# Optimization experiments

Measured on AMD Instinct MI355X. Metric: run time of the kernel, lower is better.

## Reference

```python
import jax, jax.numpy as jnp
import numpy as np

N_NODES = 100000
N_EDGES = 3200000
D_NODE = 5            # per-node feature dim
D_IN = 2 * D_NODE     # 10, MLP input dim
D_HID = D_IN * 5      # 50, HIDDEN_DIM_MULTIPLIER = 5


def setup_inputs() -> dict:
    key = jax.random.key(0)
    ks = jax.random.split(key, 8)
    x = jax.random.normal(ks[0], (N_NODES, D_NODE), dtype=jnp.float32)
    edge_index = jax.random.randint(ks[1], (2, N_EDGES), 0, N_NODES, dtype=jnp.int64)
    s1 = 1.0 / np.sqrt(D_IN)
    s2 = 1.0 / np.sqrt(D_HID)
    W1 = jax.random.uniform(ks[2], (D_IN, D_HID), jnp.float32, -s1, s1)
    b1 = jax.random.uniform(ks[3], (D_HID,), jnp.float32, -s1, s1)
    W2 = jax.random.uniform(ks[4], (D_HID, D_HID), jnp.float32, -s2, s2)
    b2 = jax.random.uniform(ks[5], (D_HID,), jnp.float32, -s2, s2)
    W3 = jax.random.uniform(ks[6], (D_HID, 1), jnp.float32, -s2, s2)
    b3 = jax.random.uniform(ks[7], (1,), jnp.float32, -s2, s2)
    return {"x": x, "edge_index": edge_index, "W1": W1, "b1": b1,
            "W2": W2, "b2": b2, "W3": W3, "b3": b3}


def reference(x, edge_index, W1, b1, W2, b2, W3, b3):
    # gather src/tgt node features and concat -> [E, 2*D_NODE]
    ef = jnp.concatenate([x[edge_index[0]], x[edge_index[1]]], axis=-1)
    h = jax.nn.relu(ef @ W1 + b1)
    h = jax.nn.relu(h @ W2 + b2)
    return jax.nn.sigmoid(h @ W3 + b3)  # [E, 1]
```

## Files before the change

kernel.cpp:

```cpp
#include <hip/hip_runtime.h>
#include <hip/hip_bf16.h>

typedef short bf16x8 __attribute__((ext_vector_type(8)));
typedef float f32x4  __attribute__((ext_vector_type(4)));

union fragU { f32x4 f; bf16x8 b; uint4 q; uint u[4]; };

__device__ inline ushort f2bf(float f) {
    union { float f; uint u; } v; v.f = f;
    uint r = (v.u + 0x7FFFu + ((v.u >> 16) & 1u)) >> 16;
    return (ushort)r;
}
__device__ inline uint packbf(float a, float b) {
    return (uint)f2bf(a) | ((uint)f2bf(b) << 16);
}
__device__ inline uint cvtpk(float lo, float hi) {
    uint r;
    asm("v_cvt_pk_bf16_f32 %0, %1, %2" : "=v"(r) : "v"(lo), "v"(hi));
    return r;
}

__global__ __launch_bounds__(256) void pack_x_kernel(
    const float* __restrict__ x, uint4* __restrict__ xp, int N)
{
    int i = blockIdx.x * blockDim.x + threadIdx.x;
    if (i > N) return;
    uint4 o = {0u, 0u, 0u, 0u};
    if (i < N) {
        const float* r = x + (size_t)i * 5;
        o.x = packbf(r[0], r[1]);
        o.y = packbf(r[2], r[3]);
        o.z = packbf(r[4], 1.0f);
    }
    xp[i] = o;
}

__global__ __launch_bounds__(64) void pack_w_kernel(
    const float* __restrict__ W1, const float* __restrict__ b1,
    const float* __restrict__ W2, const float* __restrict__ b2,
    const float* __restrict__ W3, uint4* __restrict__ tab)
{
    const int lane = threadIdx.x;
    const int c = lane & 15;
    const int g = lane >> 4;

    union { ushort s[8]; uint4 q; } u;
    #pragma unroll
    for (int mt = 0; mt < 4; ++mt) {
        #pragma unroll
        for (int d = 0; d < 8; ++d) {
            int k = 8 * g + d;
            int j = 16 * mt + c;
            float v = 0.f;
            if (j < 50) {
                if (k < 5)                 v = W1[k * 50 + j];
                else if (k == 5)           v = b1[j];
                else if (k >= 8 && k < 13) v = W1[(k - 3) * 50 + j];
            } else if (j == 50 && k == 5)  v = 1.0f;
            u.s[d] = f2bf(v);
        }
        tab[mt * 64 + lane] = u.q;
    }
    #pragma unroll
    for (int t = 0; t < 2; ++t) {
        #pragma unroll
        for (int mt = 0; mt < 4; ++mt) {
            #pragma unroll
            for (int d = 0; d < 8; ++d) {
                int hid1 = 16 * (2 * t + (d >> 2)) + 4 * g + (d & 3);
                int j    = 16 * mt + c;
                float v = 0.f;
                if (j < 50) {
                    if (hid1 < 50)       v = W2[hid1 * 50 + j];
                    else if (hid1 == 50) v = b2[j];
                }
                u.s[d] = f2bf(v);
            }
            tab[(4 + t * 4 + mt) * 64 + lane] = u.q;
        }
    }
    #pragma unroll
    for (int t = 0; t < 2; ++t) {
        #pragma unroll
        for (int d = 0; d < 8; ++d) {
            int hid = 16 * (2 * t + (d >> 2)) + 4 * g + (d & 3);
            float v = (c == 0 && hid < 50) ? W3[hid] : 0.f;
            u.s[d] = f2bf(v);
        }
        tab[(12 + t) * 64 + lane] = u.q;
    }
}

__global__ __launch_bounds__(256, 4) void edge_mlp_mfma9(
    const uint4* __restrict__ xp,
    const uint4* __restrict__ wtab,
    const int* __restrict__ ei,
    const float* __restrict__ b3,
    float* __restrict__ out, int E, int num_tiles)
{
    const int tid  = threadIdx.x;
    const int w    = tid >> 6;
    const int lane = tid & 63;
    const int c    = lane & 15;
    const int g    = lane >> 4;
    const int G    = gridDim.x;

    fragU w1f[4], w2f[8], w3f[2];
    #pragma unroll
    for (int i = 0; i < 4; ++i) w1f[i].q = wtab[i * 64 + lane];
    #pragma unroll
    for (int i = 0; i < 8; ++i) w2f[i].q = wtab[(4 + i) * 64 + lane];
    #pragma unroll
    for (int i = 0; i < 2; ++i) w3f[i].q = wtab[(12 + i) * 64 + lane];
    asm volatile("" :
        "+v"(w1f[0].f), "+v"(w1f[1].f), "+v"(w1f[2].f), "+v"(w1f[3].f),
        "+v"(w2f[0].f), "+v"(w2f[1].f), "+v"(w2f[2].f), "+v"(w2f[3].f),
        "+v"(w2f[4].f), "+v"(w2f[5].f), "+v"(w2f[6].f), "+v"(w2f[7].f),
        "+v"(w3f[0].f), "+v"(w3f[1].f));

    const float b3s = b3[0];

    auto LOAD_IDX = [&](int bt_) -> int {
        int bc = (bt_ < num_tiles) ? bt_ : (num_tiles - 1);
        int v = 0;
        if (g < 2) {
            int e = bc * 64 + w * 16 + c;
            if (e >= E) e = 0;
            v = ei[(size_t)g * (size_t)E + (size_t)e];
        }
        return v;
    };
    auto GATHER = [&](int idx) -> fragU {
        fragU a;
        uint4 q = {0u, 0u, 0u, 0u};
        if (g < 2) q = xp[idx];
        a.q = q;
        return a;
    };

    int bt = blockIdx.x;
    if (bt >= num_tiles) return;

    fragU fC = GATHER(LOAD_IDX(bt));
    int idxN = LOAD_IDX(bt + G);

    for (; bt < num_tiles; bt += G) {
        fragU fN = GATHER(idxN);
        idxN = LOAD_IDX(bt + 2 * G);

        f32x4 hT[4];
        #pragma unroll
        for (int mt = 0; mt < 4; ++mt) {
            f32x4 z = {0.f, 0.f, 0.f, 0.f};
            hT[mt] = __builtin_amdgcn_mfma_f32_16x16x32_bf16(w1f[mt].b, fC.b, z, 0, 0, 0);
        }
        fragU bB0, bB1;
        #pragma unroll
        for (int mt = 0; mt < 2; ++mt) {
            bB0.u[2*mt]   = cvtpk(fmaxf(hT[mt][0], 0.f),   fmaxf(hT[mt][1], 0.f));
            bB0.u[2*mt+1] = cvtpk(fmaxf(hT[mt][2], 0.f),   fmaxf(hT[mt][3], 0.f));
            bB1.u[2*mt]   = cvtpk(fmaxf(hT[2+mt][0], 0.f), fmaxf(hT[2+mt][1], 0.f));
            bB1.u[2*mt+1] = cvtpk(fmaxf(hT[2+mt][2], 0.f), fmaxf(hT[2+mt][3], 0.f));
        }

        f32x4 h2T[4];
        #pragma unroll
        for (int mt = 0; mt < 4; ++mt) {
            f32x4 z = {0.f, 0.f, 0.f, 0.f};
            h2T[mt] = __builtin_amdgcn_mfma_f32_16x16x32_bf16(w2f[mt].b,     bB0.b, z, 0, 0, 0);
            h2T[mt] = __builtin_amdgcn_mfma_f32_16x16x32_bf16(w2f[4 + mt].b, bB1.b, h2T[mt], 0, 0, 0);
        }
        fragU cB0, cB1;
        #pragma unroll
        for (int mt = 0; mt < 2; ++mt) {
            cB0.u[2*mt]   = cvtpk(fmaxf(h2T[mt][0], 0.f),   fmaxf(h2T[mt][1], 0.f));
            cB0.u[2*mt+1] = cvtpk(fmaxf(h2T[mt][2], 0.f),   fmaxf(h2T[mt][3], 0.f));
            cB1.u[2*mt]   = cvtpk(fmaxf(h2T[2+mt][0], 0.f), fmaxf(h2T[2+mt][1], 0.f));
            cB1.u[2*mt+1] = cvtpk(fmaxf(h2T[2+mt][2], 0.f), fmaxf(h2T[2+mt][3], 0.f));
        }

        f32x4 z3 = {0.f, 0.f, 0.f, 0.f};
        f32x4 o3 = __builtin_amdgcn_mfma_f32_16x16x32_bf16(w3f[0].b, cB0.b, z3, 0, 0, 0);
        o3 = __builtin_amdgcn_mfma_f32_16x16x32_bf16(w3f[1].b, cB1.b, o3, 0, 0, 0);

        if (g == 0) {
            int e = bt * 64 + w * 16 + c;
            if (e < E) {
                float ex = __expf(-(o3[0] + b3s));
                out[e] = __builtin_amdgcn_rcpf(1.f + ex);
            }
        }

        fC = fN;
    }
}

extern "C" void kernel_launch(void* const* d_in, const int* in_sizes, int n_in,
                              void* d_out, int out_size, void* d_ws, size_t ws_size,
                              hipStream_t stream) {
    const float* x  = (const float*)d_in[0];
    const int*   ei = (const int*)d_in[1];
    const float* W1 = (const float*)d_in[2];
    const float* b1 = (const float*)d_in[3];
    const float* W2 = (const float*)d_in[4];
    const float* b2 = (const float*)d_in[5];
    const float* W3 = (const float*)d_in[6];
    const float* b3 = (const float*)d_in[7];
    float* out = (float*)d_out;

    int E = in_sizes[1] / 2;
    int N = in_sizes[0] / 5;

    uint4* wtab = (uint4*)d_ws;
    uint4* xp   = (uint4*)((char*)d_ws + 16384);

    pack_w_kernel<<<1, 64, 0, stream>>>(W1, b1, W2, b2, W3, wtab);
    pack_x_kernel<<<(N + 1 + 255) / 256, 256, 0, stream>>>(x, xp, N);

    int num_tiles = (E + 63) / 64;
    int grid = num_tiles < 2048 ? num_tiles : 2048;
    edge_mlp_mfma9<<<grid, 256, 0, stream>>>(xp, wtab, ei, b3, out, E, num_tiles);
}
```

Baseline: 77.29 us.

## Deepen gather prefetch pipeline to four tiles and use nontemporal index loads and stores

Replaces the single-tile-ahead prefetch with a four-slot rotating buffer, so each wavefront keeps several index loads and feature gathers in flight while it runs the MFMA chain on an earlier tile. The goal is to hide gather latency in this memory-bound edge MLP. Edge index loads and output stores also become nontemporal, so streamed data does not evict the gathered node table from cache. The cost is more live registers and some wasted compute on clamped tiles at the end of the grid-stride loop, since tail tiles past num_tiles are computed and then discarded by the bounds check.

```diff
diff --git a/kernel.cpp b/kernel.cpp
--- a/kernel.cpp
+++ b/kernel.cpp
@@ -91,7 +91,7 @@
     }
 }
 
-__global__ __launch_bounds__(256, 4) void edge_mlp_mfma9(
+__global__ __launch_bounds__(256, 4) void edge_mlp_mfma10(
     const uint4* __restrict__ xp,
     const uint4* __restrict__ wtab,
     const int* __restrict__ ei,
@@ -126,7 +126,7 @@
         if (g < 2) {
             int e = bc * 64 + w * 16 + c;
             if (e >= E) e = 0;
-            v = ei[(size_t)g * (size_t)E + (size_t)e];
+            v = __builtin_nontemporal_load(&ei[(size_t)g * (size_t)E + (size_t)e]);
         }
         return v;
     };
@@ -138,21 +138,12 @@
         return a;
     };
 
-    int bt = blockIdx.x;
-    if (bt >= num_tiles) return;
-
-    fragU fC = GATHER(LOAD_IDX(bt));
-    int idxN = LOAD_IDX(bt + G);
-
-    for (; bt < num_tiles; bt += G) {
-        fragU fN = GATHER(idxN);
-        idxN = LOAD_IDX(bt + 2 * G);
-
+    auto COMPUTE = [&](fragU aX, int T) {
         f32x4 hT[4];
         #pragma unroll
         for (int mt = 0; mt < 4; ++mt) {
             f32x4 z = {0.f, 0.f, 0.f, 0.f};
-            hT[mt] = __builtin_amdgcn_mfma_f32_16x16x32_bf16(w1f[mt].b, fC.b, z, 0, 0, 0);
+            hT[mt] = __builtin_amdgcn_mfma_f32_16x16x32_bf16(w1f[mt].b, aX.b, z, 0, 0, 0);
         }
         fragU bB0, bB1;
         #pragma unroll
@@ -162,7 +153,6 @@
             bB1.u[2*mt]   = cvtpk(fmaxf(hT[2+mt][0], 0.f), fmaxf(hT[2+mt][1], 0.f));
             bB1.u[2*mt+1] = cvtpk(fmaxf(hT[2+mt][2], 0.f), fmaxf(hT[2+mt][3], 0.f));
         }
-
         f32x4 h2T[4];
         #pragma unroll
         for (int mt = 0; mt < 4; ++mt) {
@@ -178,20 +168,40 @@
             cB1.u[2*mt]   = cvtpk(fmaxf(h2T[2+mt][0], 0.f), fmaxf(h2T[2+mt][1], 0.f));
             cB1.u[2*mt+1] = cvtpk(fmaxf(h2T[2+mt][2], 0.f), fmaxf(h2T[2+mt][3], 0.f));
         }
-
         f32x4 z3 = {0.f, 0.f, 0.f, 0.f};
         f32x4 o3 = __builtin_amdgcn_mfma_f32_16x16x32_bf16(w3f[0].b, cB0.b, z3, 0, 0, 0);
         o3 = __builtin_amdgcn_mfma_f32_16x16x32_bf16(w3f[1].b, cB1.b, o3, 0, 0, 0);
 
         if (g == 0) {
-            int e = bt * 64 + w * 16 + c;
+            int e = T * 64 + w * 16 + c;
             if (e < E) {
                 float ex = __expf(-(o3[0] + b3s));
-                out[e] = __builtin_amdgcn_rcpf(1.f + ex);
+                float sg = __builtin_amdgcn_rcpf(1.f + ex);
+                __builtin_nontemporal_store(sg, &out[e]);
             }
         }
-
-        fC = fN;
+    };
+
+    int bt = blockIdx.x;
+    if (bt >= num_tiles) return;
+
+    int idxB[4];
+    fragU fB[4];
+    #pragma unroll
+    for (int p = 0; p < 4; ++p) idxB[p] = LOAD_IDX(bt + p * G);
+    #pragma unroll
+    for (int p = 0; p < 4; ++p) fB[p] = GATHER(idxB[p]);
+    #pragma unroll
+    for (int p = 0; p < 4; ++p) idxB[p] = LOAD_IDX(bt + (p + 4) * G);
+
+    for (; bt < num_tiles; bt += 4 * G) {
+        #pragma unroll
+        for (int p = 0; p < 4; ++p) {
+            const int T = bt + p * G;
+            COMPUTE(fB[p], T);
+            fB[p] = GATHER(idxB[p]);
+            idxB[p] = LOAD_IDX(bt + (p + 8) * G);
+        }
     }
 }
 
@@ -219,5 +229,5 @@
 
     int num_tiles = (E + 63) / 64;
     int grid = num_tiles < 2048 ? num_tiles : 2048;
-    edge_mlp_mfma9<<<grid, 256, 0, stream>>>(xp, wtab, ei, b3, out, E, num_tiles);
-}
+    edge_mlp_mfma10<<<grid, 256, 0, stream>>>(xp, wtab, ei, b3, out, E, num_tiles);
+}
```

Result: faster. 73.18 us (-5.3%).

## Process eight edge subtiles per wave with vectorized nontemporal index loads

Applied to the files above, without the earlier changes.

Each block now handles 512 edges per iteration instead of 64. Each lane loads 8 contiguous edge indices with two 16-byte nontemporal loads, issues 8 independent feature gathers up front, then runs the MFMA MLP chain for each subtile. This is meant to raise memory-level parallelism and cut per-edge index-load instruction overhead. It also adds s_setprio around the MFMA section, nontemporal output stores, and lowers the occupancy hint to 3 blocks per CU, at the cost of more registers and strided output writes.

```diff
diff --git a/kernel.cpp b/kernel.cpp
--- a/kernel.cpp
+++ b/kernel.cpp
@@ -3,6 +3,7 @@
 
 typedef short bf16x8 __attribute__((ext_vector_type(8)));
 typedef float f32x4  __attribute__((ext_vector_type(4)));
+typedef int   i32x4  __attribute__((ext_vector_type(4)));
 
 union fragU { f32x4 f; bf16x8 b; uint4 q; uint u[4]; };
 
@@ -91,12 +92,12 @@
     }
 }
 
-__global__ __launch_bounds__(256, 4) void edge_mlp_mfma9(
+__global__ __launch_bounds__(256, 3) void edge_mlp_mfma11(
     const uint4* __restrict__ xp,
     const uint4* __restrict__ wtab,
     const int* __restrict__ ei,
     const float* __restrict__ b3,
-    float* __restrict__ out, int E, int num_tiles)
+    float* __restrict__ out, int E, int NB)
 {
     const int tid  = threadIdx.x;
     const int w    = tid >> 6;
@@ -119,79 +120,101 @@
         "+v"(w3f[0].f), "+v"(w3f[1].f));
 
     const float b3s = b3[0];
-
-    auto LOAD_IDX = [&](int bt_) -> int {
-        int bc = (bt_ < num_tiles) ? bt_ : (num_tiles - 1);
-        int v = 0;
+    const bool e_al = ((E & 3) == 0);
+
+    auto LOAD_IDX = [&](int bt_, i32x4& a, i32x4& b) {
+        a = i32x4{0, 0, 0, 0};
+        b = i32x4{0, 0, 0, 0};
+        int bc = (bt_ < NB) ? bt_ : (NB - 1);
+        int base = bc * 512 + w * 128;
         if (g < 2) {
-            int e = bc * 64 + w * 16 + c;
-            if (e >= E) e = 0;
-            v = ei[(size_t)g * (size_t)E + (size_t)e];
-        }
-        return v;
+            if (e_al && base + 128 <= E) {
+                const i32x4* p = (const i32x4*)(ei + (size_t)g * (size_t)E + base + c * 8);
+                a = __builtin_nontemporal_load(p);
+                b = __builtin_nontemporal_load(p + 1);
+            } else {
+                int t[8];
+                #pragma unroll
+                for (int jj = 0; jj < 8; ++jj) {
+                    int e = base + c * 8 + jj;
+                    if (e >= E) e = 0;
+                    t[jj] = ei[(size_t)g * (size_t)E + (size_t)e];
+                }
+                a = i32x4{t[0], t[1], t[2], t[3]};
+                b = i32x4{t[4], t[5], t[6], t[7]};
+            }
+        }
     };
-    auto GATHER = [&](int idx) -> fragU {
-        fragU a;
-        uint4 q = {0u, 0u, 0u, 0u};
-        if (g < 2) q = xp[idx];
-        a.q = q;
-        return a;
-    };
 
     int bt = blockIdx.x;
-    if (bt >= num_tiles) return;
-
-    fragU fC = GATHER(LOAD_IDX(bt));
-    int idxN = LOAD_IDX(bt + G);
-
-    for (; bt < num_tiles; bt += G) {
-        fragU fN = GATHER(idxN);
-        idxN = LOAD_IDX(bt + 2 * G);
-
-        f32x4 hT[4];
-        #pragma unroll
-        for (int mt = 0; mt < 4; ++mt) {
-            f32x4 z = {0.f, 0.f, 0.f, 0.f};
-            hT[mt] = __builtin_amdgcn_mfma_f32_16x16x32_bf16(w1f[mt].b, fC.b, z, 0, 0, 0);
-        }
-        fragU bB0, bB1;
-        #pragma unroll
-        for (int mt = 0; mt < 2; ++mt) {
-            bB0.u[2*mt]   = cvtpk(fmaxf(hT[mt][0], 0.f),   fmaxf(hT[mt][1], 0.f));
-            bB0.u[2*mt+1] = cvtpk(fmaxf(hT[mt][2], 0.f),   fmaxf(hT[mt][3], 0.f));
-            bB1.u[2*mt]   = cvtpk(fmaxf(hT[2+mt][0], 0.f), fmaxf(hT[2+mt][1], 0.f));
-            bB1.u[2*mt+1] = cvtpk(fmaxf(hT[2+mt][2], 0.f), fmaxf(hT[2+mt][3], 0.f));
-        }
-
-        f32x4 h2T[4];
-        #pragma unroll
-        for (int mt = 0; mt < 4; ++mt) {
-            f32x4 z = {0.f, 0.f, 0.f, 0.f};
-            h2T[mt] = __builtin_amdgcn_mfma_f32_16x16x32_bf16(w2f[mt].b,     bB0.b, z, 0, 0, 0);
-            h2T[mt] = __builtin_amdgcn_mfma_f32_16x16x32_bf16(w2f[4 + mt].b, bB1.b, h2T[mt], 0, 0, 0);
-        }
-        fragU cB0, cB1;
-        #pragma unroll
-        for (int mt = 0; mt < 2; ++mt) {
-            cB0.u[2*mt]   = cvtpk(fmaxf(h2T[mt][0], 0.f),   fmaxf(h2T[mt][1], 0.f));
-            cB0.u[2*mt+1] = cvtpk(fmaxf(h2T[mt][2], 0.f),   fmaxf(h2T[mt][3], 0.f));
-            cB1.u[2*mt]   = cvtpk(fmaxf(h2T[2+mt][0], 0.f), fmaxf(h2T[2+mt][1], 0.f));
-            cB1.u[2*mt+1] = cvtpk(fmaxf(h2T[2+mt][2], 0.f), fmaxf(h2T[2+mt][3], 0.f));
-        }
-
-        f32x4 z3 = {0.f, 0.f, 0.f, 0.f};
-        f32x4 o3 = __builtin_amdgcn_mfma_f32_16x16x32_bf16(w3f[0].b, cB0.b, z3, 0, 0, 0);
-        o3 = __builtin_amdgcn_mfma_f32_16x16x32_bf16(w3f[1].b, cB1.b, o3, 0, 0, 0);
-
-        if (g == 0) {
-            int e = bt * 64 + w * 16 + c;
-            if (e < E) {
-                float ex = __expf(-(o3[0] + b3s));
-                out[e] = __builtin_amdgcn_rcpf(1.f + ex);
-            }
-        }
-
-        fC = fN;
+    if (bt >= NB) return;
+
+    i32x4 iaC, ibC, iaN, ibN;
+    LOAD_IDX(bt, iaC, ibC);
+
+    for (; bt < NB; bt += G) {
+        LOAD_IDX(bt + G, iaN, ibN);
+
+        int idxs[8] = {iaC[0], iaC[1], iaC[2], iaC[3], ibC[0], ibC[1], ibC[2], ibC[3]};
+
+        fragU f[8];
+        #pragma unroll
+        for (int j = 0; j < 8; ++j) {
+            uint4 q = {0u, 0u, 0u, 0u};
+            if (g < 2) q = xp[idxs[j]];
+            f[j].q = q;
+        }
+
+        const int base = bt * 512 + w * 128;
+
+        #pragma unroll
+        for (int j = 0; j < 8; ++j) {
+            __builtin_amdgcn_s_setprio(1);
+            f32x4 hT[4];
+            #pragma unroll
+            for (int mt = 0; mt < 4; ++mt) {
+                f32x4 z = {0.f, 0.f, 0.f, 0.f};
+                hT[mt] = __builtin_amdgcn_mfma_f32_16x16x32_bf16(w1f[mt].b, f[j].b, z, 0, 0, 0);
+            }
+            fragU bB0, bB1;
+            #pragma unroll
+            for (int mt = 0; mt < 2; ++mt) {
+                bB0.u[2*mt]   = cvtpk(fmaxf(hT[mt][0], 0.f),   fmaxf(hT[mt][1], 0.f));
+                bB0.u[2*mt+1] = cvtpk(fmaxf(hT[mt][2], 0.f),   fmaxf(hT[mt][3], 0.f));
+                bB1.u[2*mt]   = cvtpk(fmaxf(hT[2+mt][0], 0.f), fmaxf(hT[2+mt][1], 0.f));
+                bB1.u[2*mt+1] = cvtpk(fmaxf(hT[2+mt][2], 0.f), fmaxf(hT[2+mt][3], 0.f));
+            }
+            f32x4 h2T[4];
+            #pragma unroll
+            for (int mt = 0; mt < 4; ++mt) {
+                f32x4 z = {0.f, 0.f, 0.f, 0.f};
+                h2T[mt] = __builtin_amdgcn_mfma_f32_16x16x32_bf16(w2f[mt].b,     bB0.b, z, 0, 0, 0);
+                h2T[mt] = __builtin_amdgcn_mfma_f32_16x16x32_bf16(w2f[4 + mt].b, bB1.b, h2T[mt], 0, 0, 0);
+            }
+            fragU cB0, cB1;
+            #pragma unroll
+            for (int mt = 0; mt < 2; ++mt) {
+                cB0.u[2*mt]   = cvtpk(fmaxf(h2T[mt][0], 0.f),   fmaxf(h2T[mt][1], 0.f));
+                cB0.u[2*mt+1] = cvtpk(fmaxf(h2T[mt][2], 0.f),   fmaxf(h2T[mt][3], 0.f));
+                cB1.u[2*mt]   = cvtpk(fmaxf(h2T[2+mt][0], 0.f), fmaxf(h2T[2+mt][1], 0.f));
+                cB1.u[2*mt+1] = cvtpk(fmaxf(h2T[2+mt][2], 0.f), fmaxf(h2T[2+mt][3], 0.f));
+            }
+            f32x4 z3 = {0.f, 0.f, 0.f, 0.f};
+            f32x4 o3 = __builtin_amdgcn_mfma_f32_16x16x32_bf16(w3f[0].b, cB0.b, z3, 0, 0, 0);
+            o3 = __builtin_amdgcn_mfma_f32_16x16x32_bf16(w3f[1].b, cB1.b, o3, 0, 0, 0);
+            __builtin_amdgcn_s_setprio(0);
+
+            if (g == 0) {
+                int e = base + c * 8 + j;
+                if (e < E) {
+                    float ex = __expf(-(o3[0] + b3s));
+                    float sg = __builtin_amdgcn_rcpf(1.f + ex);
+                    __builtin_nontemporal_store(sg, &out[e]);
+                }
+            }
+        }
+
+        iaC = iaN; ibC = ibN;
     }
 }
 
@@ -217,7 +240,7 @@
     pack_w_kernel<<<1, 64, 0, stream>>>(W1, b1, W2, b2, W3, wtab);
     pack_x_kernel<<<(N + 1 + 255) / 256, 256, 0, stream>>>(x, xp, N);
 
-    int num_tiles = (E + 63) / 64;
-    int grid = num_tiles < 2048 ? num_tiles : 2048;
-    edge_mlp_mfma9<<<grid, 256, 0, stream>>>(xp, wtab, ei, b3, out, E, num_tiles);
-}
+    int NB = (E + 511) / 512;
+    int grid = NB < 2048 ? NB : 2048;
+    edge_mlp_mfma11<<<grid, 256, 0, stream>>>(xp, wtab, ei, b3, out, E, NB);
+}
```

Result: faster. 75.60 us (-2.2%).

## Switch edge MLP to 32x32x16 MFMA tiles with permlane swap and FMA output layer

Applied to the files above, without the earlier changes.

Each wave now processes 32 edges per tile instead of 16, using 32x32x16 bf16 MFMA for layers 1 and 2. The layer-1 accumulators are reshaped into B operands with v_permlane32_swap rather than reused directly. The final 50->1 layer becomes a per-lane FMA dot product plus a cross-half shuffle, replacing two mostly zero MFMAs. This cuts wasted MFMA work and halves the index-load and gather instructions per edge, at the cost of more registers (occupancy hint lowered from 4 to 3) and added permute and FMA instructions.

```diff
diff --git a/kernel.cpp b/kernel.cpp
--- a/kernel.cpp
+++ b/kernel.cpp
@@ -3,6 +3,7 @@
 
 typedef short bf16x8 __attribute__((ext_vector_type(8)));
 typedef float f32x4  __attribute__((ext_vector_type(4)));
+typedef float f32x16 __attribute__((ext_vector_type(16)));
 
 union fragU { f32x4 f; bf16x8 b; uint4 q; uint u[4]; };
 
@@ -24,14 +25,13 @@
     const float* __restrict__ x, uint4* __restrict__ xp, int N)
 {
     int i = blockIdx.x * blockDim.x + threadIdx.x;
-    if (i > N) return;
-    uint4 o = {0u, 0u, 0u, 0u};
-    if (i < N) {
-        const float* r = x + (size_t)i * 5;
-        o.x = packbf(r[0], r[1]);
-        o.y = packbf(r[2], r[3]);
-        o.z = packbf(r[4], 1.0f);
-    }
+    if (i >= N) return;
+    const float* r = x + (size_t)i * 5;
+    uint4 o;
+    o.x = packbf(r[0], r[1]);
+    o.y = packbf(r[2], r[3]);
+    o.z = packbf(r[4], 1.0f);
+    o.w = 0u;
     xp[i] = o;
 }
 
@@ -41,16 +41,16 @@
     const float* __restrict__ W3, uint4* __restrict__ tab)
 {
     const int lane = threadIdx.x;
-    const int c = lane & 15;
-    const int g = lane >> 4;
+    const int col  = lane & 31;
+    const int hi   = lane >> 5;
 
     union { ushort s[8]; uint4 q; } u;
     #pragma unroll
-    for (int mt = 0; mt < 4; ++mt) {
+    for (int T = 0; T < 2; ++T) {
         #pragma unroll
         for (int d = 0; d < 8; ++d) {
-            int k = 8 * g + d;
-            int j = 16 * mt + c;
+            int k = 8 * hi + d;
+            int j = 32 * T + col;
             float v = 0.f;
             if (j < 50) {
                 if (k < 5)                 v = W1[k * 50 + j];
@@ -59,139 +59,139 @@
             } else if (j == 50 && k == 5)  v = 1.0f;
             u.s[d] = f2bf(v);
         }
-        tab[mt * 64 + lane] = u.q;
-    }
-    #pragma unroll
-    for (int t = 0; t < 2; ++t) {
-        #pragma unroll
-        for (int mt = 0; mt < 4; ++mt) {
+        tab[T * 64 + lane] = u.q;
+    }
+    #pragma unroll
+    for (int T = 0; T < 2; ++T) {
+        #pragma unroll
+        for (int s = 0; s < 4; ++s) {
             #pragma unroll
             for (int d = 0; d < 8; ++d) {
-                int hid1 = 16 * (2 * t + (d >> 2)) + 4 * g + (d & 3);
-                int j    = 16 * mt + c;
+                int kg = 16 * s + 8 * hi + d;
+                int j  = 32 * T + col;
                 float v = 0.f;
                 if (j < 50) {
-                    if (hid1 < 50)       v = W2[hid1 * 50 + j];
-                    else if (hid1 == 50) v = b2[j];
+                    if (kg < 50)       v = W2[kg * 50 + j];
+                    else if (kg == 50) v = b2[j];
                 }
                 u.s[d] = f2bf(v);
             }
-            tab[(4 + t * 4 + mt) * 64 + lane] = u.q;
-        }
-    }
-    #pragma unroll
-    for (int t = 0; t < 2; ++t) {
-        #pragma unroll
-        for (int d = 0; d < 8; ++d) {
-            int hid = 16 * (2 * t + (d >> 2)) + 4 * g + (d & 3);
-            float v = (c == 0 && hid < 50) ? W3[hid] : 0.f;
-            u.s[d] = f2bf(v);
-        }
-        tab[(12 + t) * 64 + lane] = u.q;
-    }
-}
-
-__global__ __launch_bounds__(256, 4) void edge_mlp_mfma9(
+            tab[(2 + T * 4 + s) * 64 + lane] = u.q;
+        }
+    }
+    union { float f[4]; uint4 q; } wq;
+    #pragma unroll
+    for (int T = 0; T < 2; ++T) {
+        #pragma unroll
+        for (int rq = 0; rq < 4; ++rq) {
+            #pragma unroll
+            for (int rr = 0; rr < 4; ++rr) {
+                int reg = 4 * rq + rr;
+                int row = (reg & 3) + 8 * (reg >> 2) + 4 * hi + 32 * T;
+                wq.f[rr] = (row < 50) ? W3[row] : 0.f;
+            }
+            tab[(10 + T * 4 + rq) * 64 + lane] = wq.q;
+        }
+    }
+}
+
+__global__ __launch_bounds__(256, 3) void edge_mlp_mfma12(
     const uint4* __restrict__ xp,
     const uint4* __restrict__ wtab,
     const int* __restrict__ ei,
     const float* __restrict__ b3,
-    float* __restrict__ out, int E, int num_tiles)
+    float* __restrict__ out, int E, int NT)
 {
     const int tid  = threadIdx.x;
     const int w    = tid >> 6;
     const int lane = tid & 63;
-    const int c    = lane & 15;
-    const int g    = lane >> 4;
+    const int col  = lane & 31;
+    const int hi   = lane >> 5;
     const int G    = gridDim.x;
 
-    fragU w1f[4], w2f[8], w3f[2];
-    #pragma unroll
-    for (int i = 0; i < 4; ++i) w1f[i].q = wtab[i * 64 + lane];
-    #pragma unroll
-    for (int i = 0; i < 8; ++i) w2f[i].q = wtab[(4 + i) * 64 + lane];
-    #pragma unroll
-    for (int i = 0; i < 2; ++i) w3f[i].q = wtab[(12 + i) * 64 + lane];
+    fragU w1f[2], w2f[8], w3q[8];
+    #pragma unroll
+    for (int i = 0; i < 2; ++i) w1f[i].q = wtab[i * 64 + lane];
+    #pragma unroll
+    for (int i = 0; i < 8; ++i) w2f[i].q = wtab[(2 + i) * 64 + lane];
+    #pragma unroll
+    for (int i = 0; i < 8; ++i) w3q[i].q = wtab[(10 + i) * 64 + lane];
     asm volatile("" :
-        "+v"(w1f[0].f), "+v"(w1f[1].f), "+v"(w1f[2].f), "+v"(w1f[3].f),
+        "+v"(w1f[0].f), "+v"(w1f[1].f),
         "+v"(w2f[0].f), "+v"(w2f[1].f), "+v"(w2f[2].f), "+v"(w2f[3].f),
         "+v"(w2f[4].f), "+v"(w2f[5].f), "+v"(w2f[6].f), "+v"(w2f[7].f),
-        "+v"(w3f[0].f), "+v"(w3f[1].f));
+        "+v"(w3q[0].f), "+v"(w3q[1].f), "+v"(w3q[2].f), "+v"(w3q[3].f),
+        "+v"(w3q[4].f), "+v"(w3q[5].f), "+v"(w3q[6].f), "+v"(w3q[7].f));
 
     const float b3s = b3[0];
 
-    auto LOAD_IDX = [&](int bt_) -> int {
-        int bc = (bt_ < num_tiles) ? bt_ : (num_tiles - 1);
-        int v = 0;
-        if (g < 2) {
-            int e = bc * 64 + w * 16 + c;
-            if (e >= E) e = 0;
-            v = ei[(size_t)g * (size_t)E + (size_t)e];
-        }
-        return v;
+    auto LOAD_IDX = [&](int t_) -> int {
+        int tc = (t_ < NT) ? t_ : (NT - 1);
+        int e = tc * 128 + w * 32 + col;
+        if (e >= E) e = 0;
+        return ei[(size_t)hi * (size_t)E + (size_t)e];
     };
-    auto GATHER = [&](int idx) -> fragU {
-        fragU a;
-        uint4 q = {0u, 0u, 0u, 0u};
-        if (g < 2) q = xp[idx];
-        a.q = q;
-        return a;
-    };
-
-    int bt = blockIdx.x;
-    if (bt >= num_tiles) return;
-
-    fragU fC = GATHER(LOAD_IDX(bt));
-    int idxN = LOAD_IDX(bt + G);
-
-    for (; bt < num_tiles; bt += G) {
-        fragU fN = GATHER(idxN);
-        idxN = LOAD_IDX(bt + 2 * G);
-
-        f32x4 hT[4];
-        #pragma unroll
-        for (int mt = 0; mt < 4; ++mt) {
-            f32x4 z = {0.f, 0.f, 0.f, 0.f};
-            hT[mt] = __builtin_amdgcn_mfma_f32_16x16x32_bf16(w1f[mt].b, fC.b, z, 0, 0, 0);
-        }
-        fragU bB0, bB1;
-        #pragma unroll
-        for (int mt = 0; mt < 2; ++mt) {
-            bB0.u[2*mt]   = cvtpk(fmaxf(hT[mt][0], 0.f),   fmaxf(hT[mt][1], 0.f));
-            bB0.u[2*mt+1] = cvtpk(fmaxf(hT[mt][2], 0.f),   fmaxf(hT[mt][3], 0.f));
-            bB1.u[2*mt]   = cvtpk(fmaxf(hT[2+mt][0], 0.f), fmaxf(hT[2+mt][1], 0.f));
-            bB1.u[2*mt+1] = cvtpk(fmaxf(hT[2+mt][2], 0.f), fmaxf(hT[2+mt][3], 0.f));
-        }
-
-        f32x4 h2T[4];
-        #pragma unroll
-        for (int mt = 0; mt < 4; ++mt) {
-            f32x4 z = {0.f, 0.f, 0.f, 0.f};
-            h2T[mt] = __builtin_amdgcn_mfma_f32_16x16x32_bf16(w2f[mt].b,     bB0.b, z, 0, 0, 0);
-            h2T[mt] = __builtin_amdgcn_mfma_f32_16x16x32_bf16(w2f[4 + mt].b, bB1.b, h2T[mt], 0, 0, 0);
-        }
-        fragU cB0, cB1;
-        #pragma unroll
-        for (int mt = 0; mt < 2; ++mt) {
-            cB0.u[2*mt]   = cvtpk(fmaxf(h2T[mt][0], 0.f),   fmaxf(h2T[mt][1], 0.f));
-            cB0.u[2*mt+1] = cvtpk(fmaxf(h2T[mt][2], 0.f),   fmaxf(h2T[mt][3], 0.f));
-            cB1.u[2*mt]   = cvtpk(fmaxf(h2T[2+mt][0], 0.f), fmaxf(h2T[2+mt][1], 0.f));
-            cB1.u[2*mt+1] = cvtpk(fmaxf(h2T[2+mt][2], 0.f), fmaxf(h2T[2+mt][3], 0.f));
-        }
-
-        f32x4 z3 = {0.f, 0.f, 0.f, 0.f};
-        f32x4 o3 = __builtin_amdgcn_mfma_f32_16x16x32_bf16(w3f[0].b, cB0.b, z3, 0, 0, 0);
-        o3 = __builtin_amdgcn_mfma_f32_16x16x32_bf16(w3f[1].b, cB1.b, o3, 0, 0, 0);
-
-        if (g == 0) {
-            int e = bt * 64 + w * 16 + c;
+
+    const f32x16 z16 = {0.f,0.f,0.f,0.f, 0.f,0.f,0.f,0.f,
+                        0.f,0.f,0.f,0.f, 0.f,0.f,0.f,0.f};
+
+    int t = blockIdx.x;
+    if (t >= NT) return;
+
+    fragU f0; f0.q = xp[LOAD_IDX(t)];
+    int idx1 = LOAD_IDX(t + G);
+
+    for (; t < NT; t += G) {
+        fragU f1; f1.q = xp[idx1];
+        idx1 = LOAD_IDX(t + 2 * G);
+
+        f32x16 c1_0 = __builtin_amdgcn_mfma_f32_32x32x16_bf16(w1f[0].b, f0.b, z16, 0, 0, 0);
+        f32x16 c1_1 = __builtin_amdgcn_mfma_f32_32x32x16_bf16(w1f[1].b, f0.b, z16, 0, 0, 0);
+
+        uint word[2][8];
+        #pragma unroll
+        for (int k = 0; k < 8; ++k) {
+            word[0][k] = cvtpk(fmaxf(c1_0[2*k], 0.f), fmaxf(c1_0[2*k+1], 0.f));
+            word[1][k] = cvtpk(fmaxf(c1_1[2*k], 0.f), fmaxf(c1_1[2*k+1], 0.f));
+        }
+        fragU bf[4];
+        #pragma unroll
+        for (int s = 0; s < 4; ++s) {
+            #pragma unroll
+            for (int n = 0; n < 2; ++n) {
+                const int mD = 2 * s, mS = 2 * s + 1;
+                uint D = word[mD >> 2][2 * (mD & 3) + n];
+                uint S = word[mS >> 2][2 * (mS & 3) + n];
+                asm volatile("v_permlane32_swap_b32 %0, %1" : "+v"(D), "+v"(S));
+                bf[s].u[n]     = D;
+                bf[s].u[2 + n] = S;
+            }
+        }
+
+        f32x16 c2_0 = z16, c2_1 = z16;
+        #pragma unroll
+        for (int s = 0; s < 4; ++s) {
+            c2_0 = __builtin_amdgcn_mfma_f32_32x32x16_bf16(w2f[s].b,     bf[s].b, c2_0, 0, 0, 0);
+            c2_1 = __builtin_amdgcn_mfma_f32_32x32x16_bf16(w2f[4 + s].b, bf[s].b, c2_1, 0, 0, 0);
+        }
+
+        float p = 0.f;
+        #pragma unroll
+        for (int reg = 0; reg < 16; ++reg) {
+            p = fmaf(fmaxf(c2_0[reg], 0.f), w3q[reg >> 2].f[reg & 3], p);
+            p = fmaf(fmaxf(c2_1[reg], 0.f), w3q[4 + (reg >> 2)].f[reg & 3], p);
+        }
+        p += __shfl_xor(p, 32);
+
+        if (hi == 0) {
+            int e = t * 128 + w * 32 + col;
             if (e < E) {
-                float ex = __expf(-(o3[0] + b3s));
+                float ex = __expf(-(p + b3s));
                 out[e] = __builtin_amdgcn_rcpf(1.f + ex);
             }
         }
 
-        fC = fN;
+        f0 = f1;
     }
 }
 
@@ -212,12 +212,12 @@
     int N = in_sizes[0] / 5;
 
     uint4* wtab = (uint4*)d_ws;
-    uint4* xp   = (uint4*)((char*)d_ws + 16384);
+    uint4* xp   = (uint4*)((char*)d_ws + 32768);
 
     pack_w_kernel<<<1, 64, 0, stream>>>(W1, b1, W2, b2, W3, wtab);
-    pack_x_kernel<<<(N + 1 + 255) / 256, 256, 0, stream>>>(x, xp, N);
-
-    int num_tiles = (E + 63) / 64;
-    int grid = num_tiles < 2048 ? num_tiles : 2048;
-    edge_mlp_mfma9<<<grid, 256, 0, stream>>>(xp, wtab, ei, b3, out, E, num_tiles);
-}
+    pack_x_kernel<<<(N + 255) / 256, 256, 0, stream>>>(x, xp, N);
+
+    int NT = (E + 127) / 128;
+    int grid = NT < 2048 ? NT : 2048;
+    edge_mlp_mfma12<<<grid, 256, 0, stream>>>(xp, wtab, ei, b3, out, E, NT);
+}
```

New measurement: 65.82 us. 14.8% less time.
